# Kernel tuning notes

Measured on AMD Instinct MI355X. Metric: run time of the kernel, lower is better.

## Reference

```python
import jax, jax.numpy as jnp
import numpy as np

D_MODEL, D_STATE, EXPAND = 1024, 16, 2
D_INNER = EXPAND * D_MODEL
BATCH, SEQ = 4, 4096


def setup_inputs() -> dict:
    key = jax.random.key(0)
    ks = jax.random.split(key, 9)
    s = 0.02
    return {
        "x": jax.random.normal(ks[0], (BATCH, SEQ, D_MODEL), jnp.float32),
        # torch Linear weight [out,in] stored transposed here as [in,out]
        "W_in": jax.random.normal(ks[1], (D_MODEL, 2 * D_INNER), jnp.float32) * s,
        "conv_w": jax.random.normal(ks[2], (D_INNER, 1, 3), jnp.float32) * s,  # depthwise, groups=D_INNER
        "conv_b": jax.random.normal(ks[3], (D_INNER,), jnp.float32) * s,
        "W_B": jax.random.normal(ks[4], (D_INNER, D_STATE), jnp.float32) * s,
        "W_C": jax.random.normal(ks[5], (D_INNER, D_STATE), jnp.float32) * s,
        "A": jax.random.normal(ks[6], (D_STATE,), jnp.float32),
        "D": jnp.ones((D_INNER,), jnp.float32),
        "W_out": jax.random.normal(ks[7], (D_INNER, D_MODEL), jnp.float32) * s,
    }


def reference(x, W_in, conv_w, conv_b, W_B, W_C, A, D, W_out):
    d_inner = conv_w.shape[0]
    # input projection and split into main / residual gate paths
    xr = jnp.einsum("bld,de->ble", x, W_in)  # [B, L, 2*d_inner]
    x_main, res = xr[..., :d_inner], xr[..., d_inner:]
    # depthwise conv1d along seq (kernel 3, pad 1)
    xc = jax.lax.conv_general_dilated(
        x_main.transpose(0, 2, 1), conv_w, (1,), [(1, 1)],
        dimension_numbers=("NCH", "OIH", "NCH"), feature_group_count=d_inner)
    xc = (xc + conv_b[None, :, None]).transpose(0, 2, 1)  # [B, L, d_inner]
    xc = jax.nn.silu(xc)
    # selective-scan inputs
    Bt = jnp.einsum("bli,is->bls", xc, W_B)  # [B, L, d_state]
    Ct = jnp.einsum("bli,is->bls", xc, W_C)
    decay = jnp.exp(-jax.nn.softplus(A))  # exp(A_diag), [d_state]

    def step(state, bc):
        b_t, c_t = bc
        state = state * decay + b_t  # i=0: zeros*decay + B[0] == B[0]
        return state, jnp.sum(state * c_t, axis=-1)  # scalar per batch

    _, ys = jax.lax.scan(step, jnp.zeros_like(Bt[:, 0]),
                         (Bt.transpose(1, 0, 2), Ct.transpose(1, 0, 2)))
    ys = ys.T  # [B, L]
    y = ys[..., None] + xc * D  # broadcast scan output across d_inner
    y = y * jax.nn.silu(res)
    return jnp.einsum("bli,id->bld", y, W_out)
```

## Files before the change

kernel.cpp:

```cpp
#include <hip/hip_runtime.h>


typedef _Float16 half8 __attribute__((ext_vector_type(8)));
typedef float floatx4 __attribute__((ext_vector_type(4)));

#define D_MODEL 1024
#define D_INNER 2048
#define SEQ     4096
#define NBATCH  4
#define NROWS   (NBATCH * SEQ)
#define CHUNK   16
#define NCHUNK  (SEQ / CHUNK)
#define NTASK   (NBATCH * NCHUNK)

__device__ __forceinline__ void async16(_Float16* lds, const _Float16* g) {
    __builtin_amdgcn_global_load_lds((const __attribute__((address_space(1))) void*)g,
                                     (__attribute__((address_space(3))) void*)lds, 16, 0, 0);
}

__device__ __forceinline__ float siluf(float x) {
    return x / (1.f + __expf(-x));
}

__device__ __forceinline__ float decay_of(const float* A, int s) {
    return __expf(-log1pf(__expf(A[s])));
}


__global__ __launch_bounds__(256) void convert_f32_f16(const float* __restrict__ src,
                                                       _Float16* __restrict__ dst) {
    size_t idx = ((size_t)blockIdx.x * 256 + threadIdx.x) * 8;
    float4 a = *(const float4*)(src + idx);
    float4 b = *(const float4*)(src + idx + 4);
    half8 o = {(_Float16)a.x, (_Float16)a.y, (_Float16)a.z, (_Float16)a.w,
               (_Float16)b.x, (_Float16)b.y, (_Float16)b.z, (_Float16)b.w};
    *(half8*)(dst + idx) = o;
}

__global__ __launch_bounds__(256) void transpose_to_f16(const float* __restrict__ src,
                                                        _Float16* __restrict__ dst,
                                                        int K, int N) {
    __shared__ float tile[32][33];
    int n0 = blockIdx.x * 32, k0 = blockIdx.y * 32;
    int x = threadIdx.x, y = threadIdx.y;
#pragma unroll
    for (int r = 0; r < 32; r += 8)
        tile[y + r][x] = src[(size_t)(k0 + y + r) * N + (n0 + x)];
    __syncthreads();
#pragma unroll
    for (int r = 0; r < 32; r += 8)
        dst[(size_t)(n0 + y + r) * K + (k0 + x)] = (_Float16)tile[x][y + r];
}

__global__ __launch_bounds__(256) void convert_wbct(const float* __restrict__ WB,
                                                    const float* __restrict__ WC,
                                                    _Float16* __restrict__ WBCT) {
    int idx = blockIdx.x * 256 + threadIdx.x;
    int n = idx >> 11, k = idx & 2047;
    float v = (n < 16) ? WB[k * 16 + n] : WC[k * 16 + (n - 16)];
    WBCT[idx] = (_Float16)v;
}


__device__ __forceinline__ void stage_half(const _Float16* __restrict__ src, int K,
                                           int rowBase, int k0, _Float16* ldsHalf) {
    const int tid = threadIdx.x;
    const int sr = tid >> 3, wid = tid >> 6;
    const int lc = ((tid & 7) ^ (sr & 7)) << 3;
#pragma unroll
    for (int r = 0; r < 2; r++) {
        const _Float16* g = src + (size_t)(rowBase + r * 64 + sr) * K + (k0 + lc);
        async16(ldsHalf + r * 4096 + wid * 512, g);
    }
}

__device__ __forceinline__ void loadA8(half8 af[4][2], const _Float16* p,
                                       int sw0, int sw1) {
#pragma unroll
    for (int m = 0; m < 4; m++) {
        af[m][0] = *(const half8*)(p + m * 1024 + sw0);
        af[m][1] = *(const half8*)(p + m * 1024 + sw1);
    }
}

__device__ __forceinline__ void loadB4(half8 bf[2][2], const _Float16* p,
                                       int sw0, int sw1) {
#pragma unroll
    for (int n = 0; n < 2; n++) {
        bf[n][0] = *(const half8*)(p + n * 1024 + sw0);
        bf[n][1] = *(const half8*)(p + n * 1024 + sw1);
    }
}

#define GP_MMA(CB, BF)                                                                  \
    __builtin_amdgcn_s_barrier();                                                       \
    __builtin_amdgcn_s_setprio(1);                                                      \
    _Pragma("unroll") for (int m = 0; m < 4; m++)                                       \
        _Pragma("unroll") for (int n = 0; n < 2; n++)                                   \
            _Pragma("unroll") for (int s = 0; s < 2; s++)                               \
                acc[m][(CB) * 2 + n] = __builtin_amdgcn_mfma_f32_16x16x32_f16(          \
                    af[m][s], (BF)[n][s], acc[m][(CB) * 2 + n], 0, 0, 0);               \
    __builtin_amdgcn_s_setprio(0);                                                      \
    __builtin_amdgcn_s_barrier();

template <typename OutT>
__global__ __launch_bounds__(512, 2) void gemm256(const _Float16* __restrict__ A,
                                                  const _Float16* __restrict__ BT,
                                                  OutT* __restrict__ C,
                                                  int M, int N, int K) {
    __shared__ __align__(16) _Float16 smem[4 * 16384];
    _Float16* const AsBase = smem;
    _Float16* const BsBase = smem + 32768;

    const int tid = threadIdx.x;
    const int wid = tid >> 6, lane = tid & 63;
    const int wm = wid >> 1, wn = wid & 1;
    const int fr = lane & 15, q = lane >> 4, frq = fr & 7;
    const int sw0 = (q ^ frq) << 3;
    const int sw1 = ((4 + q) ^ frq) << 3;
    const int aB0 = (wm * 64 + fr) * 64;
    const int bB0 = (wn * 128 + fr) * 64;

    int lin = blockIdx.y * gridDim.x + blockIdx.x;
    const int nwg = gridDim.x * gridDim.y;
    lin = (lin & 7) * (nwg >> 3) + (lin >> 3);
    const int bx = lin % gridDim.x, by = lin / gridDim.x;
    const int row0 = by * 256, col0 = bx * 256;
    const int NT = K >> 6;

    floatx4 acc[4][8] = {};
    half8 af[4][2], bfA[2][2], bfB[2][2];

    stage_half(A,  K, row0,       0, AsBase);
    stage_half(A,  K, row0 + 128, 0, AsBase + 8192);
    stage_half(BT, K, col0,       0, BsBase);
    stage_half(BT, K, col0 + 128, 0, BsBase + 8192);
    if (NT > 1) {
        stage_half(A, K, row0, 64, AsBase + 16384);
        asm volatile("s_waitcnt vmcnt(2)" ::: "memory");
    } else {
        asm volatile("s_waitcnt vmcnt(0)" ::: "memory");
    }
    __builtin_amdgcn_s_barrier();
    asm volatile("" ::: "memory");
    loadB4(bfA, BsBase + bB0, sw0, sw1);
    loadA8(af, AsBase + aB0, sw0, sw1);

    for (int t = 0; t < NT; ++t) {
        _Float16* Ab  = AsBase + ((t & 1) << 14);
        _Float16* Bb  = BsBase + ((t & 1) << 14);
        _Float16* Abn = AsBase + (((t + 1) & 1) << 14);
        _Float16* Bbn = BsBase + (((t + 1) & 1) << 14);
        const int k1 = (t + 1) << 6, k2 = (t + 2) << 6;
        const bool s1 = (t + 1) < NT, s2 = (t + 2) < NT;

        loadB4(bfB, Bb + bB0 + 2048, sw0, sw1);
        if (s1) {
            stage_half(A,  K, row0 + 128, k1, Abn + 8192);
            stage_half(BT, K, col0,       k1, Bbn);
        }
        GP_MMA(0, bfA);

        loadB4(bfA, Bb + bB0 + 4096, sw0, sw1);
        if (s1) stage_half(BT, K, col0 + 128, k1, Bbn + 8192);
        GP_MMA(1, bfB);

        loadB4(bfB, Bb + bB0 + 6144, sw0, sw1);
        if (s2) stage_half(A, K, row0, k2, Ab);
        GP_MMA(2, bfA);

        if (s2) {
            asm volatile("s_waitcnt vmcnt(2)" ::: "memory");
        } else if (s1) {
            asm volatile("s_waitcnt vmcnt(0)" ::: "memory");
        }
        __builtin_amdgcn_s_barrier();
        asm volatile("" ::: "memory");
        if (s1) loadB4(bfA, Bbn + bB0, sw0, sw1);
        __builtin_amdgcn_s_setprio(1);
#pragma unroll
        for (int m = 0; m < 4; m++)
#pragma unroll
            for (int n = 0; n < 2; n++)
#pragma unroll
                for (int s = 0; s < 2; s++)
                    acc[m][6 + n] = __builtin_amdgcn_mfma_f32_16x16x32_f16(
                        af[m][s], bfB[n][s], acc[m][6 + n], 0, 0, 0);
        __builtin_amdgcn_s_setprio(0);
        if (s1) loadA8(af, Abn + aB0, sw0, sw1);
        __builtin_amdgcn_s_barrier();
    }

    const int er = (lane >> 4) * 4, ec = lane & 15;
#pragma unroll
    for (int mi = 0; mi < 4; mi++)
#pragma unroll
        for (int cj = 0; cj < 8; cj++)
#pragma unroll
            for (int r = 0; r < 4; r++) {
                int row = row0 + wm * 64 + mi * 16 + er + r;
                int col = col0 + wn * 128 + cj * 16 + ec;
                C[(size_t)row * N + col] = (OutT)acc[mi][cj][r];
            }
}

__global__ __launch_bounds__(256) void conv_bc_fin(const _Float16* __restrict__ xr,
                                                   const float* __restrict__ cw,
                                                   const float* __restrict__ cb,
                                                   const _Float16* __restrict__ WBCT,
                                                   const float* __restrict__ A,
                                                   _Float16* __restrict__ xc,
                                                   float* __restrict__ BtCt,
                                                   float* __restrict__ fin) {
    __shared__ __align__(16) _Float16 As[4 * 32 * 128];
    const int tid = threadIdx.x, wid = tid >> 6, lane = tid & 63;
    const int row0 = blockIdx.x * 32;
    const int l0 = row0 & (SEQ - 1);
    const int cg = lane & 15;
    const int rg = lane >> 4;
    const int fr = lane & 15, q = lane >> 4;
    _Float16* As_w = As + wid * 4096;
    const int r0 = rg * 8;

    floatx4 acc[2][2] = {};

    for (int t = 0; t < 4; t++) {
        const int kbase = wid * 512 + t * 128;
        const int gcol = kbase + cg * 8;
        float w0[8], w1[8], w2[8], bb[8];
#pragma unroll
        for (int j = 0; j < 8; j++) {
            w0[j] = cw[(gcol + j) * 3];
            w1[j] = cw[(gcol + j) * 3 + 1];
            w2[j] = cw[(gcol + j) * 3 + 2];
            bb[j] = cb[gcol + j];
        }
        half8 prev = {}, cur, nxt;
        if (!(l0 == 0 && rg == 0))
            prev = *(const half8*)(xr + (size_t)(row0 + r0 - 1) * 4096 + gcol);
        cur = *(const half8*)(xr + (size_t)(row0 + r0) * 4096 + gcol);
#pragma unroll
        for (int r = 0; r < 8; r++) {
            if (r == 7 && rg == 3 && l0 + 32 == SEQ) {
                half8 z = {};
                nxt = z;
            } else {
                nxt = *(const half8*)(xr + (size_t)(row0 + r0 + r + 1) * 4096 + gcol);
            }
            half8 o;
#pragma unroll
            for (int j = 0; j < 8; j++) {
                float a = (float)prev[j] * w0[j] + (float)cur[j] * w1[j] +
                          (float)nxt[j] * w2[j] + bb[j];
                o[j] = (_Float16)siluf(a);
            }
            const int lrow = r0 + r;
            *(half8*)(xc + (size_t)(row0 + lrow) * D_INNER + gcol) = o;
            *(half8*)(As_w + lrow * 128 + ((cg ^ (lrow & 7)) * 8)) = o;
            prev = cur;
            cur = nxt;
        }
#pragma unroll
        for (int ks = 0; ks < 4; ks++) {
            half8 af[2], bf[2];
#pragma unroll
            for (int rt = 0; rt < 2; rt++)
                af[rt] = *(const half8*)(As_w + (rt * 16 + fr) * 128 +
                                         (((ks * 4 + q) ^ (fr & 7)) * 8));
#pragma unroll
            for (int ot = 0; ot < 2; ot++)
                bf[ot] = *(const half8*)(WBCT + (size_t)(ot * 16 + fr) * D_INNER +
                                         kbase + ks * 32 + q * 8);
#pragma unroll
            for (int rt = 0; rt < 2; rt++)
#pragma unroll
                for (int ot = 0; ot < 2; ot++)
                    acc[rt][ot] = __builtin_amdgcn_mfma_f32_16x16x32_f16(af[rt], bf[ot], acc[rt][ot], 0, 0, 0);
        }
    }

    __syncthreads();
    float* red = (float*)As;
    float* btl = (float*)As + 4096;
    const int er = (lane >> 4) * 4, ec = lane & 15;
#pragma unroll
    for (int rt = 0; rt < 2; rt++)
#pragma unroll
        for (int ot = 0; ot < 2; ot++)
#pragma unroll
            for (int rr = 0; rr < 4; rr++)
                red[wid * 1024 + (rt * 16 + er + rr) * 32 + ot * 16 + ec] = acc[rt][ot][rr];
    __syncthreads();
#pragma unroll
    for (int i = 0; i < 4; i++) {
        int idx = i * 256 + tid;
        float v = red[idx] + red[1024 + idx] + red[2048 + idx] + red[3072 + idx];
        btl[idx] = v;
        BtCt[(size_t)row0 * 32 + idx] = v;
    }
    __syncthreads();
    if (tid < 32) {
        const int ch = tid >> 4, s = tid & 15;
        const float decay = decay_of(A, s);
        float st = 0.f;
#pragma unroll
        for (int r = 0; r < CHUNK; r++)
            st = st * decay + btl[(ch * 16 + r) * 32 + s];
        fin[((row0 >> 4) + ch) * 16 + s] = st;
    }
}

__global__ __launch_bounds__(64) void scan_p2(const float* __restrict__ fin,
                                              const float* __restrict__ A,
                                              float* __restrict__ carry) {
    int t = threadIdx.x;
    int b = t >> 4, s = t & 15;
    float decay = decay_of(A, s);
    float d16 = decay;
#pragma unroll
    for (int k = 0; k < 4; k++) d16 *= d16;
    float cy = 0.f;
#pragma unroll 8
    for (int c = 0; c < NCHUNK; c++) {
        int idx = ((b * NCHUNK) + c) * 16 + s;
        carry[idx] = cy;
        cy = cy * d16 + fin[idx];
    }
}

__global__ __launch_bounds__(256) void scan_p3_fuse(const float* __restrict__ BtCt,
                                                    const float* __restrict__ A,
                                                    const float* __restrict__ carry,
                                                    const float* __restrict__ D,
                                                    const _Float16* __restrict__ xr,
                                                    _Float16* __restrict__ xc) {
    __shared__ float ysl[CHUNK];
    const int task = blockIdx.x;
    const int b = task >> 8, c = task & (NCHUNK - 1);
    const int row0 = b * SEQ + c * CHUNK;
    const int tid = threadIdx.x;

    if (tid < 16) {
        const int s = tid;
        const float decay = decay_of(A, s);
        size_t r = (size_t)row0 * 32;
        float bt[CHUNK], ct[CHUNK];
#pragma unroll
        for (int j = 0; j < CHUNK; j++) {
            bt[j] = BtCt[r + (size_t)j * 32 + s];
            ct[j] = BtCt[r + (size_t)j * 32 + 16 + s];
        }
        float st = carry[task * 16 + s];
        float yv[CHUNK];
#pragma unroll
        for (int j = 0; j < CHUNK; j++) {
            st = st * decay + bt[j];
            yv[j] = st * ct[j];
        }
#pragma unroll
        for (int j = 0; j < CHUNK; j++) {
            float y = yv[j];
            y += __shfl_xor(y, 1, 16);
            y += __shfl_xor(y, 2, 16);
            y += __shfl_xor(y, 4, 16);
            y += __shfl_xor(y, 8, 16);
            if (s == 0) ysl[j] = y;
        }
    }
    __syncthreads();

#pragma unroll
    for (int it = 0; it < 16; it++) {
        int chunk = it * 256 + tid;
        int rl = chunk >> 8;
        int colb = (chunk & 255) * 8;
        size_t row = (size_t)(row0 + rl);
        float yv = ysl[rl];
        half8 x8 = *(const half8*)(xc + row * D_INNER + colb);
        half8 r8 = *(const half8*)(xr + row * 4096 + 2048 + colb);
        float4 d0 = *(const float4*)(D + colb);
        float4 d1 = *(const float4*)(D + colb + 4);
        half8 o;
        float dd[8] = {d0.x, d0.y, d0.z, d0.w, d1.x, d1.y, d1.z, d1.w};
#pragma unroll
        for (int j = 0; j < 8; j++) {
            float y = yv + (float)x8[j] * dd[j];
            o[j] = (_Float16)(y * siluf((float)r8[j]));
        }
        *(half8*)(xc + row * D_INNER + colb) = o;
    }
}

extern "C" void kernel_launch(void* const* d_in, const int* in_sizes, int n_in,
                              void* d_out, int out_size, void* d_ws, size_t ws_size,
                              hipStream_t stream) {
    const float* x      = (const float*)d_in[0];
    const float* W_in   = (const float*)d_in[1];
    const float* conv_w = (const float*)d_in[2];
    const float* conv_b = (const float*)d_in[3];
    const float* W_B    = (const float*)d_in[4];
    const float* W_C    = (const float*)d_in[5];
    const float* A      = (const float*)d_in[6];
    const float* D      = (const float*)d_in[7];
    const float* W_out  = (const float*)d_in[8];
    float* out = (float*)d_out;

    char* ws = (char*)d_ws;
    size_t off = 0;
    auto alloc = [&](size_t bytes) { size_t o = off; off += (bytes + 255) & ~(size_t)255; return o; };
    _Float16* xh    = (_Float16*)(ws + alloc((size_t)NROWS * D_MODEL * 2));
    _Float16* WinT  = (_Float16*)(ws + alloc((size_t)4096 * 1024 * 2));
    _Float16* WoutT = (_Float16*)(ws + alloc((size_t)1024 * 2048 * 2));
    _Float16* WBCT  = (_Float16*)(ws + alloc((size_t)32 * 2048 * 2));
    _Float16* xr    = (_Float16*)(ws + alloc((size_t)NROWS * 4096 * 2));
    _Float16* xc    = (_Float16*)(ws + alloc((size_t)NROWS * D_INNER * 2));
    float*    BtCt  = (float*)(ws + alloc((size_t)NROWS * 32 * 4));
    float*    fin   = (float*)(ws + alloc((size_t)NTASK * 16 * 4));
    float*    carry = (float*)(ws + alloc((size_t)NTASK * 16 * 4));

    convert_f32_f16<<<(NROWS * D_MODEL) / (256 * 8), 256, 0, stream>>>(x, xh);
    transpose_to_f16<<<dim3(4096 / 32, 1024 / 32), dim3(32, 8), 0, stream>>>(W_in, WinT, 1024, 4096);
    transpose_to_f16<<<dim3(1024 / 32, 2048 / 32), dim3(32, 8), 0, stream>>>(W_out, WoutT, 2048, 1024);
    convert_wbct<<<(32 * 2048) / 256, 256, 0, stream>>>(W_B, W_C, WBCT);
    gemm256<_Float16><<<dim3(4096 / 256, NROWS / 256), 512, 0, stream>>>(xh, WinT, xr, NROWS, 4096, 1024);
    conv_bc_fin<<<NROWS / 32, 256, 0, stream>>>(xr, conv_w, conv_b, WBCT, A, xc, BtCt, fin);
    scan_p2<<<1, 64, 0, stream>>>(fin, A, carry);
    scan_p3_fuse<<<NTASK, 256, 0, stream>>>(BtCt, A, carry, D, xr, xc);
    gemm256<float><<<dim3(1024 / 256, NROWS / 256), 512, 0, stream>>>(xc, WoutT, out, NROWS, 1024, 2048);
}
```

Measured before the change: 448.9 us.

## Make input GEMM persistent over multiple row tiles and reorder MFMA loops

```diff
diff --git a/kernel.cpp b/kernel.cpp
--- a/kernel.cpp
+++ b/kernel.cpp
@@ -95,15 +95,15 @@
 #define GP_MMA(CB, BF)                                                                  \
     __builtin_amdgcn_s_barrier();                                                       \
     __builtin_amdgcn_s_setprio(1);                                                      \
-    _Pragma("unroll") for (int m = 0; m < 4; m++)                                       \
-        _Pragma("unroll") for (int n = 0; n < 2; n++)                                   \
-            _Pragma("unroll") for (int s = 0; s < 2; s++)                               \
+    _Pragma("unroll") for (int s = 0; s < 2; s++)                                       \
+        _Pragma("unroll") for (int m = 0; m < 4; m++)                                   \
+            _Pragma("unroll") for (int n = 0; n < 2; n++)                               \
                 acc[m][(CB) * 2 + n] = __builtin_amdgcn_mfma_f32_16x16x32_f16(          \
                     af[m][s], (BF)[n][s], acc[m][(CB) * 2 + n], 0, 0, 0);               \
     __builtin_amdgcn_s_setprio(0);                                                      \
     __builtin_amdgcn_s_barrier();
 
-template <typename OutT>
+template <typename OutT, int NC, int RT>
 __global__ __launch_bounds__(512, 2) void gemm256(const _Float16* __restrict__ A,
                                                   const _Float16* __restrict__ BT,
                                                   OutT* __restrict__ C,
@@ -121,87 +121,99 @@
     const int aB0 = (wm * 64 + fr) * 64;
     const int bB0 = (wn * 128 + fr) * 64;
 
-    int lin = blockIdx.y * gridDim.x + blockIdx.x;
-    const int nwg = gridDim.x * gridDim.y;
-    lin = (lin & 7) * (nwg >> 3) + (lin >> 3);
-    const int bx = lin % gridDim.x, by = lin / gridDim.x;
-    const int row0 = by * 256, col0 = bx * 256;
+    const int b = blockIdx.x;
+    const int col0 = (b % NC) * 256;
+    const int rowBase = (b / NC) * (RT * 256);
     const int NT = K >> 6;
 
-    floatx4 acc[4][8] = {};
     half8 af[4][2], bfA[2][2], bfB[2][2];
 
-    stage_half(A,  K, row0,       0, AsBase);
-    stage_half(A,  K, row0 + 128, 0, AsBase + 8192);
-    stage_half(BT, K, col0,       0, BsBase);
-    stage_half(BT, K, col0 + 128, 0, BsBase + 8192);
-    if (NT > 1) {
-        stage_half(A, K, row0, 64, AsBase + 16384);
-        asm volatile("s_waitcnt vmcnt(2)" ::: "memory");
-    } else {
-        asm volatile("s_waitcnt vmcnt(0)" ::: "memory");
-    }
+    stage_half(A,  K, rowBase,       0, AsBase);
+    stage_half(A,  K, rowBase + 128, 0, AsBase + 8192);
+    stage_half(BT, K, col0,          0, BsBase);
+    stage_half(BT, K, col0 + 128,    0, BsBase + 8192);
+    stage_half(A,  K, rowBase,      64, AsBase + 16384);
+    asm volatile("s_waitcnt vmcnt(2)" ::: "memory");
     __builtin_amdgcn_s_barrier();
     asm volatile("" ::: "memory");
     loadB4(bfA, BsBase + bB0, sw0, sw1);
     loadA8(af, AsBase + aB0, sw0, sw1);
 
-    for (int t = 0; t < NT; ++t) {
-        _Float16* Ab  = AsBase + ((t & 1) << 14);
-        _Float16* Bb  = BsBase + ((t & 1) << 14);
-        _Float16* Abn = AsBase + (((t + 1) & 1) << 14);
-        _Float16* Bbn = BsBase + (((t + 1) & 1) << 14);
-        const int k1 = (t + 1) << 6, k2 = (t + 2) << 6;
-        const bool s1 = (t + 1) < NT, s2 = (t + 2) < NT;
-
-        loadB4(bfB, Bb + bB0 + 2048, sw0, sw1);
-        if (s1) {
-            stage_half(A,  K, row0 + 128, k1, Abn + 8192);
-            stage_half(BT, K, col0,       k1, Bbn);
-        }
-        GP_MMA(0, bfA);
-
-        loadB4(bfA, Bb + bB0 + 4096, sw0, sw1);
-        if (s1) stage_half(BT, K, col0 + 128, k1, Bbn + 8192);
-        GP_MMA(1, bfB);
-
-        loadB4(bfB, Bb + bB0 + 6144, sw0, sw1);
-        if (s2) stage_half(A, K, row0, k2, Ab);
-        GP_MMA(2, bfA);
-
-        if (s2) {
+    for (int rt = 0; rt < RT; ++rt) {
+        const int row0 = rowBase + rt * 256;
+        floatx4 acc[4][8] = {};
+
+        for (int t = 0; t < NT; ++t) {
+            _Float16* Ab  = AsBase + ((t & 1) << 14);
+            _Float16* Bb  = BsBase + ((t & 1) << 14);
+            _Float16* Abn = AsBase + (((t + 1) & 1) << 14);
+            _Float16* Bbn = BsBase + (((t + 1) & 1) << 14);
+            const int k1 = (t + 1) << 6, k2 = (t + 2) << 6;
+            const bool s1 = (t + 1) < NT, s2 = (t + 2) < NT;
+
+            loadB4(bfB, Bb + bB0 + 2048, sw0, sw1);
+            if (s1) {
+                stage_half(A,  K, row0 + 128, k1, Abn + 8192);
+                stage_half(BT, K, col0,       k1, Bbn);
+            }
+            GP_MMA(0, bfA);
+
+            loadB4(bfA, Bb + bB0 + 4096, sw0, sw1);
+            if (s1) stage_half(BT, K, col0 + 128, k1, Bbn + 8192);
+            GP_MMA(1, bfB);
+
+            loadB4(bfB, Bb + bB0 + 6144, sw0, sw1);
+            if (s2) stage_half(A, K, row0, k2, Ab);
+            GP_MMA(2, bfA);
+
+            if (s2) {
+                asm volatile("s_waitcnt vmcnt(2)" ::: "memory");
+            } else if (s1) {
+                asm volatile("s_waitcnt vmcnt(0)" ::: "memory");
+            }
+            __builtin_amdgcn_s_barrier();
+            asm volatile("" ::: "memory");
+            if (s1) loadB4(bfA, Bbn + bB0, sw0, sw1);
+            __builtin_amdgcn_s_setprio(1);
+#pragma unroll
+            for (int s = 0; s < 2; s++)
+#pragma unroll
+                for (int m = 0; m < 4; m++)
+#pragma unroll
+                    for (int n = 0; n < 2; n++)
+                        acc[m][6 + n] = __builtin_amdgcn_mfma_f32_16x16x32_f16(
+                            af[m][s], bfB[n][s], acc[m][6 + n], 0, 0, 0);
+            __builtin_amdgcn_s_setprio(0);
+            if (s1) loadA8(af, Abn + aB0, sw0, sw1);
+            __builtin_amdgcn_s_barrier();
+        }
+
+        if (rt + 1 < RT) {
+            const int row0n = row0 + 256;
+            stage_half(A,  K, row0n,       0, AsBase);
+            stage_half(A,  K, row0n + 128, 0, AsBase + 8192);
+            stage_half(BT, K, col0,        0, BsBase);
+            stage_half(BT, K, col0 + 128,  0, BsBase + 8192);
+            stage_half(A,  K, row0n,      64, AsBase + 16384);
             asm volatile("s_waitcnt vmcnt(2)" ::: "memory");
-        } else if (s1) {
-            asm volatile("s_waitcnt vmcnt(0)" ::: "memory");
-        }
-        __builtin_amdgcn_s_barrier();
-        asm volatile("" ::: "memory");
-        if (s1) loadB4(bfA, Bbn + bB0, sw0, sw1);
-        __builtin_amdgcn_s_setprio(1);
-#pragma unroll
-        for (int m = 0; m < 4; m++)
-#pragma unroll
-            for (int n = 0; n < 2; n++)
-#pragma unroll
-                for (int s = 0; s < 2; s++)
-                    acc[m][6 + n] = __builtin_amdgcn_mfma_f32_16x16x32_f16(
-                        af[m][s], bfB[n][s], acc[m][6 + n], 0, 0, 0);
-        __builtin_amdgcn_s_setprio(0);
-        if (s1) loadA8(af, Abn + aB0, sw0, sw1);
-        __builtin_amdgcn_s_barrier();
-    }
-
-    const int er = (lane >> 4) * 4, ec = lane & 15;
-#pragma unroll
-    for (int mi = 0; mi < 4; mi++)
-#pragma unroll
-        for (int cj = 0; cj < 8; cj++)
-#pragma unroll
-            for (int r = 0; r < 4; r++) {
-                int row = row0 + wm * 64 + mi * 16 + er + r;
-                int col = col0 + wn * 128 + cj * 16 + ec;
-                C[(size_t)row * N + col] = (OutT)acc[mi][cj][r];
-            }
+            __builtin_amdgcn_s_barrier();
+            asm volatile("" ::: "memory");
+            loadB4(bfA, BsBase + bB0, sw0, sw1);
+            loadA8(af, AsBase + aB0, sw0, sw1);
+        }
+
+        const int er = (lane >> 4) * 4, ec = lane & 15;
+#pragma unroll
+        for (int mi = 0; mi < 4; mi++)
+#pragma unroll
+            for (int cj = 0; cj < 8; cj++)
+#pragma unroll
+                for (int r = 0; r < 4; r++) {
+                    int row = row0 + wm * 64 + mi * 16 + er + r;
+                    int col = col0 + wn * 128 + cj * 16 + ec;
+                    C[(size_t)row * N + col] = (OutT)acc[mi][cj][r];
+                }
+    }
 }
 
 __global__ __launch_bounds__(256) void conv_bc_fin(const _Float16* __restrict__ xr,
@@ -422,9 +434,9 @@
     transpose_to_f16<<<dim3(4096 / 32, 1024 / 32), dim3(32, 8), 0, stream>>>(W_in, WinT, 1024, 4096);
     transpose_to_f16<<<dim3(1024 / 32, 2048 / 32), dim3(32, 8), 0, stream>>>(W_out, WoutT, 2048, 1024);
     convert_wbct<<<(32 * 2048) / 256, 256, 0, stream>>>(W_B, W_C, WBCT);
-    gemm256<_Float16><<<dim3(4096 / 256, NROWS / 256), 512, 0, stream>>>(xh, WinT, xr, NROWS, 4096, 1024);
+    gemm256<_Float16, 16, 4><<<256, 512, 0, stream>>>(xh, WinT, xr, NROWS, 4096, 1024);
     conv_bc_fin<<<NROWS / 32, 256, 0, stream>>>(xr, conv_w, conv_b, WBCT, A, xc, BtCt, fin);
     scan_p2<<<1, 64, 0, stream>>>(fin, A, carry);
     scan_p3_fuse<<<NTASK, 256, 0, stream>>>(BtCt, A, carry, D, xr, xc);
-    gemm256<float><<<dim3(1024 / 256, NROWS / 256), 512, 0, stream>>>(xc, WoutT, out, NROWS, 1024, 2048);
-}
+    gemm256<float, 4, 1><<<256, 512, 0, stream>>>(xc, WoutT, out, NROWS, 1024, 2048);
+}
```

Measured after the change: 428.1 us. 4.6% less time.
